# Optimization experiments

Hardware: AMD Instinct MI355X
Metric: run time of the kernel (lower is better)

## Reference

```python
import jax, jax.numpy as jnp
import numpy as np

N_NODES = 100000
N_EDGES = 1600000
N_GRAPHS = 1000
D_IN = 128
HID = 128
OUT = 6


def setup_inputs() -> dict:
    key = jax.random.key(0)
    ks = jax.random.split(key, 12)
    s = 1.0 / np.sqrt(HID)
    x = jax.random.normal(ks[0], (N_NODES, D_IN), dtype=jnp.float32)
    ei = jax.random.randint(ks[1], (2, N_EDGES), 0, N_NODES, dtype=jnp.int64)
    batch = jnp.sort(jax.random.randint(ks[2], (N_NODES,), 0, N_GRAPHS, dtype=jnp.int64))
    return {
        "x": x,
        "ei": ei,
        "batch": batch,
        "W1a": jax.random.normal(ks[3], (D_IN, HID), dtype=jnp.float32) * s,
        "b1a": jnp.zeros((HID,), jnp.float32),
        "W1b": jax.random.normal(ks[4], (HID, HID), dtype=jnp.float32) * s,
        "b1b": jnp.zeros((HID,), jnp.float32),
        "W2a": jax.random.normal(ks[5], (HID, HID), dtype=jnp.float32) * s,
        "b2a": jnp.zeros((HID,), jnp.float32),
        "W2b": jax.random.normal(ks[6], (HID, HID), dtype=jnp.float32) * s,
        "b2b": jnp.zeros((HID,), jnp.float32),
        "Wlin": jax.random.normal(ks[7], (HID, OUT), dtype=jnp.float32) * s,
        "blin": jnp.zeros((OUT,), jnp.float32),
    }


def _gin_conv(x, src, dst, Wa, ba, Wb, bb):
    # PyG GINConv (eps=0): mlp(x_i + sum_{j->i} x_j)
    agg = jax.ops.segment_sum(x[src], dst, num_segments=N_NODES)
    h = agg + x
    h = jnp.maximum(h @ Wa + ba, 0.0)
    return h @ Wb + bb


def reference(x, ei, batch, W1a, b1a, W1b, b1b, W2a, b2a, W2b, b2b, Wlin, blin):
    src, dst = ei[0], ei[1]
    h = jnp.maximum(_gin_conv(x, src, dst, W1a, b1a, W1b, b1b), 0.0)
    # dropout is identity in eval mode
    h = _gin_conv(h, src, dst, W2a, b2a, W2b, b2b)
    # global mean pool per graph
    sums = jax.ops.segment_sum(h, batch, num_segments=N_GRAPHS)
    cnts = jax.ops.segment_sum(jnp.ones((h.shape[0], 1), h.dtype), batch, num_segments=N_GRAPHS)
    pooled = sums / jnp.maximum(cnts, 1.0)
    return pooled @ Wlin + blin
```

## Files before the change

kernel.cpp:

```cpp
#include <hip/hip_runtime.h>

#define N_NODES 100000
#define N_EDGES 1600000
#define N_GRAPHS 1000
#define HID 128
#define OUTD 6

#define BUCK_LOG 7
#define BUCK_W (1 << BUCK_LOG)
#define NBUCK ((N_NODES + BUCK_W - 1) >> BUCK_LOG)
#define BCAP 2560
#define FILL_BLOCKS 512
#define FILL_CHUNK 3128

#define CVT_BLOCKS 6250
#define GST_BLOCKS 391
#define PACK_BLOCKS 32
#define PREP_BLOCKS (CVT_BLOCKS + GST_BLOCKS + PACK_BLOCKS + FILL_BLOCKS)

typedef _Float16 h2 __attribute__((ext_vector_type(2)));
typedef _Float16 half8 __attribute__((ext_vector_type(8)));
typedef float f32x4 __attribute__((ext_vector_type(4)));

__global__ __launch_bounds__(256) void k_prep(const float* __restrict__ x,
                                              const int* __restrict__ batch,
                                              const int* __restrict__ srcv,
                                              const int* __restrict__ dstv,
                                              const float* __restrict__ W1a,
                                              const float* __restrict__ W1b,
                                              const float* __restrict__ W2a,
                                              const float* __restrict__ W2b,
                                              _Float16* __restrict__ X16,
                                              int* __restrict__ gstart,
                                              _Float16* __restrict__ P,
                                              int* __restrict__ bcur0,
                                              int* __restrict__ packed) {
    __shared__ int h[NBUCK];
    __shared__ int lcur[NBUCK];
    __shared__ int dcache[FILL_CHUNK];
    int b = blockIdx.x, t = threadIdx.x;
    if (b < FILL_BLOCKS) {
        int e0 = b * FILL_CHUNK;
        int e1 = min(e0 + FILL_CHUNK, N_EDGES);
        for (int i = t; i < NBUCK; i += 256) h[i] = 0;
        __syncthreads();
        int ev = e0 + ((e1 - e0) & ~3);
        for (int e = e0 + t * 4; e < ev; e += 1024) {
            int4 d4 = *(const int4*)(dstv + e);
            *(int4*)&dcache[e - e0] = d4;
            atomicAdd(&h[d4.x >> BUCK_LOG], 1);
            atomicAdd(&h[d4.y >> BUCK_LOG], 1);
            atomicAdd(&h[d4.z >> BUCK_LOG], 1);
            atomicAdd(&h[d4.w >> BUCK_LOG], 1);
        }
        for (int e = ev + t; e < e1; e += 256) {
            int d = dstv[e];
            dcache[e - e0] = d;
            atomicAdd(&h[d >> BUCK_LOG], 1);
        }
        __syncthreads();
        for (int i = t; i < NBUCK; i += 256) {
            int c = h[i];
            lcur[i] = c ? atomicAdd(&bcur0[i], c) : 0;
        }
        __syncthreads();
        for (int e = e0 + t * 4; e < ev; e += 1024) {
            int4 d4 = *(const int4*)&dcache[e - e0];
            int4 s4 = *(const int4*)(srcv + e);
            int b0 = d4.x >> BUCK_LOG, b1 = d4.y >> BUCK_LOG;
            int b2 = d4.z >> BUCK_LOG, b3 = d4.w >> BUCK_LOG;
            int p0 = atomicAdd(&lcur[b0], 1);
            int p1 = atomicAdd(&lcur[b1], 1);
            int p2 = atomicAdd(&lcur[b2], 1);
            int p3 = atomicAdd(&lcur[b3], 1);
            if (p0 < BCAP) packed[b0 * BCAP + p0] = ((d4.x & (BUCK_W - 1)) << 20) | s4.x;
            if (p1 < BCAP) packed[b1 * BCAP + p1] = ((d4.y & (BUCK_W - 1)) << 20) | s4.y;
            if (p2 < BCAP) packed[b2 * BCAP + p2] = ((d4.z & (BUCK_W - 1)) << 20) | s4.z;
            if (p3 < BCAP) packed[b3 * BCAP + p3] = ((d4.w & (BUCK_W - 1)) << 20) | s4.w;
        }
        for (int e = ev + t; e < e1; e += 256) {
            int d = dcache[e - e0];
            int bk = d >> BUCK_LOG;
            int pos = atomicAdd(&lcur[bk], 1);
            if (pos < BCAP) packed[bk * BCAP + pos] = ((d & (BUCK_W - 1)) << 20) | srcv[e];
        }
    } else if (b < FILL_BLOCKS + CVT_BLOCKS) {
        size_t i = ((size_t)(b - FILL_BLOCKS) * 256 + t) * 8;
        float4 v0 = *(const float4*)(x + i);
        float4 v1 = *(const float4*)(x + i + 4);
        half8 o;
        o[0] = (_Float16)v0.x; o[1] = (_Float16)v0.y; o[2] = (_Float16)v0.z; o[3] = (_Float16)v0.w;
        o[4] = (_Float16)v1.x; o[5] = (_Float16)v1.y; o[6] = (_Float16)v1.z; o[7] = (_Float16)v1.w;
        *(half8*)(X16 + i) = o;
    } else if (b < FILL_BLOCKS + CVT_BLOCKS + GST_BLOCKS) {
        int n = (b - FILL_BLOCKS - CVT_BLOCKS) * 256 + t;
        if (n < N_NODES) {
            int bb = batch[n];
            int prev = (n == 0) ? -1 : batch[n - 1];
            for (int g = prev + 1; g <= bb; ++g) gstart[g] = n;
            if (n == N_NODES - 1)
                for (int g = bb + 1; g <= N_GRAPHS; ++g) gstart[g] = N_NODES;
        }
    } else {
        int gid = (b - FILL_BLOCKS - CVT_BLOCKS - GST_BLOCKS) * 256 + t;
        int mat = gid >> 11;
        int r = gid & 2047;
        int ctks = r >> 6;
        int lane = r & 63;
        int col = (ctks >> 2) * 16 + (lane & 15);
        int k0 = (ctks & 3) * 32 + (lane >> 4) * 8;
        const float* W = (mat == 0) ? W1a : (mat == 1) ? W1b : (mat == 2) ? W2a : W2b;
        _Float16* dp = P + mat * 16384 + r * 8;
#pragma unroll
        for (int j = 0; j < 8; ++j) dp[j] = (_Float16)W[(k0 + j) * HID + col];
    }
}

__global__ __launch_bounds__(256) void k_csrfine(const int* __restrict__ packed,
                                                 const int* __restrict__ bcur0,
                                                 int* __restrict__ offsets,
                                                 int* __restrict__ csr_src) {
    __shared__ int hist[BUCK_W];
    __shared__ int scan[BUCK_W];
    __shared__ int cur[BUCK_W];
    __shared__ int red[4];
    int b = blockIdx.x;
    int base = b << BUCK_LOG;
    int t = threadIdx.x;
    int partial = 0;
    for (int j = t; j < b; j += 256) partial += bcur0[j];
#pragma unroll
    for (int d = 32; d > 0; d >>= 1) partial += __shfl_down(partial, d, 64);
    if ((t & 63) == 0) red[t >> 6] = partial;
    __syncthreads();
    int s = red[0] + red[1] + red[2] + red[3];
    int cnt = bcur0[b];
    if (cnt > BCAP) cnt = BCAP;
    const int* pb = packed + b * BCAP;

    if (t < BUCK_W) hist[t] = 0;
    __syncthreads();
    for (int i = t; i < cnt; i += 256) atomicAdd(&hist[pb[i] >> 20], 1);
    __syncthreads();
    if (t < BUCK_W) scan[t] = hist[t];
    __syncthreads();
    for (int d = 1; d < BUCK_W; d <<= 1) {
        int a = 0;
        if (t >= d && t < BUCK_W) a = scan[t - d];
        __syncthreads();
        if (t < BUCK_W) scan[t] += a;
        __syncthreads();
    }
    if (t < BUCK_W) {
        int node = base + t;
        if (node < N_NODES) {
            int excl = scan[t] - hist[t];
            offsets[node] = s + excl;
            cur[t] = excl;
        }
    }
    if (b == 0 && t == 0) offsets[N_NODES] = N_EDGES;
    __syncthreads();
    for (int i = t; i < cnt; i += 256) {
        int v = pb[i];
        int ln = v >> 20;
        int pos = atomicAdd(&cur[ln], 1);
        csr_src[s + pos] = v & 0xFFFFF;
    }
}

static __device__ __forceinline__ half8 shfl_xor_h8(half8 v, int mask) {
    union { half8 h; int i[4]; } a, b;
    a.h = v;
#pragma unroll
    for (int k = 0; k < 4; ++k) b.i[k] = __shfl_xor(a.i[k], mask, 64);
    return b.h;
}

__global__ __launch_bounds__(256) void k_gather16(const _Float16* __restrict__ x,
                                                  const int* __restrict__ csr,
                                                  const int* __restrict__ offs,
                                                  _Float16* __restrict__ out) {
    int t = threadIdx.x;
    int wave = t >> 6, lane = t & 63;
    int g = lane >> 4;
    int l = lane & 15;
    int node = __builtin_amdgcn_readfirstlane(blockIdx.x * 4 + wave);
    const half8* xp8 = (const half8*)x;
    int s = offs[node], e = offs[node + 1];

    half8 z = {0, 0, 0, 0, 0, 0, 0, 0};
    half8 acc0 = (g == 0) ? xp8[(size_t)node * 16 + l] : z;
    half8 acc1 = z;

    for (int base = s; base < e; base += 64) {
        int cnt = e - base;
        if (cnt > 64) cnt = 64;
        int myidx = (base + lane < e) ? csr[base + lane] : 0;
        int j = 0;
        for (; j + 16 <= cnt; j += 16) {
            int i0 = __shfl(myidx, j + g, 64);
            int i1 = __shfl(myidx, j + 4 + g, 64);
            int i2 = __shfl(myidx, j + 8 + g, 64);
            int i3 = __shfl(myidx, j + 12 + g, 64);
            acc0 += xp8[(size_t)i0 * 16 + l];
            acc1 += xp8[(size_t)i1 * 16 + l];
            acc0 += xp8[(size_t)i2 * 16 + l];
            acc1 += xp8[(size_t)i3 * 16 + l];
        }
        for (; j < cnt; j += 4) {
            int sl = j + g;
            int idx = __shfl(myidx, sl < cnt ? sl : 0, 64);
            if (sl < cnt) acc0 += xp8[(size_t)idx * 16 + l];
        }
    }
    half8 r = acc0 + acc1;
    r += shfl_xor_h8(r, 16);
    r += shfl_xor_h8(r, 32);
    if (g == 0) ((half8*)out)[(size_t)node * 16 + l] = r;
}

static __device__ __forceinline__ unsigned long long pack4(float v0, float v1,
                                                           float v2, float v3) {
    union { h2 h[2]; unsigned long long u; } u;
    h2 p0, p1;
    p0[0] = (_Float16)v0; p0[1] = (_Float16)v1;
    p1[0] = (_Float16)v2; p1[1] = (_Float16)v3;
    u.h[0] = p0; u.h[1] = p1;
    return u.u;
}

template <int RELU_OUT>
__global__ __launch_bounds__(256, 2) void k_mlp16(const _Float16* __restrict__ in,
                                                  const _Float16* __restrict__ Wap,
                                                  const float* __restrict__ ba,
                                                  const _Float16* __restrict__ Wbp,
                                                  const float* __restrict__ bb,
                                                  _Float16* __restrict__ out) {
    __shared__ uint4 WaS4[2048];
    __shared__ uint4 WbS4[2048];
    __shared__ unsigned long long hS[4][512];
    int t = threadIdx.x;
    int wave = t >> 6, lane = t & 63;
    int l = lane & 15, w = lane >> 4;
    int row0 = blockIdx.x * 256 + wave * 64;

    const uint4* wa4 = (const uint4*)Wap;
    const uint4* wb4 = (const uint4*)Wbp;
#pragma unroll
    for (int i = 0; i < 8; ++i) WaS4[t + i * 256] = wa4[t + i * 256];
#pragma unroll
    for (int i = 0; i < 8; ++i) WbS4[t + i * 256] = wb4[t + i * 256];
    __syncthreads();
    const half8* waf = (const half8*)WaS4;
    const half8* wbf = (const half8*)WbS4;
    unsigned long long* h64 = hS[wave];
    int swz = ((l & 3) << 2) ^ (((l >> 2) & 1) << 1);

    float4 baR[8], bbR[8];
#pragma unroll
    for (int ct = 0; ct < 8; ++ct) {
        baR[ct] = *(const float4*)(ba + ct * 16 + w * 4);
        bbR[ct] = *(const float4*)(bb + ct * 16 + w * 4);
    }

#pragma unroll
    for (int tile = 0; tile < 4; ++tile) {
        int row = row0 + tile * 16 + l;
        bool rok = row < N_NODES;
        const _Float16* rp = in + (size_t)row * HID + w * 8;
        half8 xf[4];
#pragma unroll
        for (int ks = 0; ks < 4; ++ks) {
            half8 v = {0, 0, 0, 0, 0, 0, 0, 0};
            if (rok) v = *(const half8*)(rp + ks * 32);
            xf[ks] = v;
        }
#pragma unroll
        for (int ct = 0; ct < 8; ++ct) {
            f32x4 c = {0.f, 0.f, 0.f, 0.f};
#pragma unroll
            for (int ks = 0; ks < 4; ++ks)
                c = __builtin_amdgcn_mfma_f32_16x16x32_f16(waf[(ct * 4 + ks) * 64 + lane],
                                                           xf[ks], c, 0, 0, 0);
            float4 b4 = baR[ct];
            h64[l * 32 + ((ct * 4 + w) ^ swz)] =
                pack4(fmaxf(c[0] + b4.x, 0.f), fmaxf(c[1] + b4.y, 0.f),
                      fmaxf(c[2] + b4.z, 0.f), fmaxf(c[3] + b4.w, 0.f));
        }
        half8 hf[4];
#pragma unroll
        for (int ks = 0; ks < 4; ++ks) {
            int slot = (ks * 8 + w * 2) ^ swz;
            hf[ks] = *(const half8*)&h64[l * 32 + slot];
        }
#pragma unroll
        for (int ct = 0; ct < 8; ++ct) {
            f32x4 c = {0.f, 0.f, 0.f, 0.f};
#pragma unroll
            for (int ks = 0; ks < 4; ++ks)
                c = __builtin_amdgcn_mfma_f32_16x16x32_f16(wbf[(ct * 4 + ks) * 64 + lane],
                                                           hf[ks], c, 0, 0, 0);
            float4 b4 = bbR[ct];
            float v0 = c[0] + b4.x, v1 = c[1] + b4.y, v2 = c[2] + b4.z, v3 = c[3] + b4.w;
            if (RELU_OUT) {
                v0 = fmaxf(v0, 0.f); v1 = fmaxf(v1, 0.f);
                v2 = fmaxf(v2, 0.f); v3 = fmaxf(v3, 0.f);
            }
            if (rok)
                *(unsigned long long*)(out + (size_t)row * HID + ct * 16 + w * 4) =
                    pack4(v0, v1, v2, v3);
        }
    }
}

__global__ __launch_bounds__(256) void k_pool_head(const _Float16* __restrict__ h,
                                                   const int* __restrict__ gstart,
                                                   const float* __restrict__ Wlin,
                                                   const float* __restrict__ blin,
                                                   float* __restrict__ out) {
    __shared__ float sums[4][HID];
    int g = blockIdx.x;
    int t = threadIdx.x;
    int wave = t >> 6, lane = t & 63;
    int s = gstart[g], e = gstart[g + 1];
    float ax = 0.f, ay = 0.f;
    const h2* hp = (const h2*)h;
    int r = s + wave;
    for (; r + 12 < e; r += 16) {
        h2 v0 = hp[(size_t)r * 64 + lane];
        h2 v1 = hp[(size_t)(r + 4) * 64 + lane];
        h2 v2 = hp[(size_t)(r + 8) * 64 + lane];
        h2 v3 = hp[(size_t)(r + 12) * 64 + lane];
        ax += (float)v0[0] + (float)v1[0] + (float)v2[0] + (float)v3[0];
        ay += (float)v0[1] + (float)v1[1] + (float)v2[1] + (float)v3[1];
    }
    for (; r < e; r += 4) {
        h2 v = hp[(size_t)r * 64 + lane];
        ax += (float)v[0];
        ay += (float)v[1];
    }
    sums[wave][2 * lane] = ax;
    sums[wave][2 * lane + 1] = ay;
    __syncthreads();
    if (wave != 0) return;
    float c = fmaxf((float)(e - s), 1.0f);
    float px = (sums[0][2 * lane] + sums[1][2 * lane] + sums[2][2 * lane] + sums[3][2 * lane]) / c;
    float py = (sums[0][2 * lane + 1] + sums[1][2 * lane + 1] + sums[2][2 * lane + 1] +
                sums[3][2 * lane + 1]) / c;
#pragma unroll
    for (int o = 0; o < OUTD; ++o) {
        float v = px * Wlin[(2 * lane) * OUTD + o] + py * Wlin[(2 * lane + 1) * OUTD + o];
#pragma unroll
        for (int d = 32; d > 0; d >>= 1) v += __shfl_down(v, d, 64);
        if (lane == 0) out[g * OUTD + o] = v + blin[o];
    }
}

extern "C" void kernel_launch(void* const* d_in, const int* in_sizes, int n_in,
                              void* d_out, int out_size, void* d_ws, size_t ws_size,
                              hipStream_t stream) {
    const float* x    = (const float*)d_in[0];
    const int*   ei   = (const int*)d_in[1];
    const int*   batch= (const int*)d_in[2];
    const float* W1a  = (const float*)d_in[3];
    const float* b1a  = (const float*)d_in[4];
    const float* W1b  = (const float*)d_in[5];
    const float* b1b  = (const float*)d_in[6];
    const float* W2a  = (const float*)d_in[7];
    const float* b2a  = (const float*)d_in[8];
    const float* W2b  = (const float*)d_in[9];
    const float* b2b  = (const float*)d_in[10];
    const float* Wlin = (const float*)d_in[11];
    const float* blin = (const float*)d_in[12];
    const int* src = ei;
    const int* dst = ei + N_EDGES;
    float* out = (float*)d_out;

    char* ws = (char*)d_ws;
    size_t off = 0;
    auto alloc = [&](size_t bytes) -> void* {
        void* p = ws + off;
        off += (bytes + 255) & ~(size_t)255;
        return p;
    };
    _Float16* X16 = (_Float16*)alloc(2ull * N_NODES * HID);
    _Float16* M   = (_Float16*)alloc(2ull * N_NODES * HID + 65536);
    _Float16* H1  = (_Float16*)alloc(2ull * N_NODES * HID + 65536);
    int*   csr_src = (int*)alloc(sizeof(int) * (size_t)N_EDGES);
    int*   offsets = (int*)alloc(sizeof(int) * (N_NODES + 1));
    int*   gstart  = (int*)alloc(sizeof(int) * (N_GRAPHS + 1));
    int*   bcur0   = (int*)alloc(sizeof(int) * NBUCK);
    _Float16* Wpack = (_Float16*)alloc(2ull * 4 * 16384);
    int* packed = (int*)H1;
    _Float16* M2 = M;
    _Float16* H2 = X16;
    (void)ws_size; (void)in_sizes; (void)n_in; (void)out_size;

    hipMemsetAsync(bcur0, 0, sizeof(int) * NBUCK, stream);

    k_prep<<<PREP_BLOCKS, 256, 0, stream>>>(x, batch, src, dst, W1a, W1b, W2a, W2b,
                                            X16, gstart, Wpack, bcur0, packed);
    k_csrfine<<<NBUCK, 256, 0, stream>>>(packed, bcur0, offsets, csr_src);

    k_gather16<<<N_NODES / 4, 256, 0, stream>>>(X16, csr_src, offsets, M);
    k_mlp16<1><<<(N_NODES + 255) / 256, 256, 0, stream>>>(M, Wpack + 0 * 16384, b1a,
                                                          Wpack + 1 * 16384, b1b, H1);
    k_gather16<<<N_NODES / 4, 256, 0, stream>>>(H1, csr_src, offsets, M2);
    k_mlp16<0><<<(N_NODES + 255) / 256, 256, 0, stream>>>(M2, Wpack + 2 * 16384, b2a,
                                                          Wpack + 3 * 16384, b2b, H2);

    k_pool_head<<<N_GRAPHS, 256, 0, stream>>>(H2, gstart, Wlin, blin, out);
}
```

Before: 306.9 us.

## Fuse second GIN MLP with mean-pool via per-graph atomic accumulation

Replaces the second MLP kernel and the pooling kernel with a fused kernel that computes the layer-2 MLP and sums each row's output into a per-graph fp32 buffer. Tiles whose 16 rows share one graph are reduced with shuffles before a single atomic per column; mixed tiles fall back to per-row atomics. A small head kernel then divides by counts and applies the linear layer. This removes the write and re-read of the 100k x 128 fp16 H2 tensor. In exchange it adds atomic traffic, a larger memset and nondeterministic summation order.

```diff
diff --git a/kernel.cpp b/kernel.cpp
--- a/kernel.cpp
+++ b/kernel.cpp
@@ -314,40 +314,127 @@
     }
 }
 
-__global__ __launch_bounds__(256) void k_pool_head(const _Float16* __restrict__ h,
-                                                   const int* __restrict__ gstart,
-                                                   const float* __restrict__ Wlin,
-                                                   const float* __restrict__ blin,
-                                                   float* __restrict__ out) {
-    __shared__ float sums[4][HID];
-    int g = blockIdx.x;
+__global__ __launch_bounds__(256, 2) void k_mlp2pool(const _Float16* __restrict__ in,
+                                                     const _Float16* __restrict__ Wap,
+                                                     const float* __restrict__ ba,
+                                                     const _Float16* __restrict__ Wbp,
+                                                     const float* __restrict__ bb,
+                                                     const int* __restrict__ batch,
+                                                     float* __restrict__ pooled) {
+    __shared__ uint4 WaS4[2048];
+    __shared__ uint4 WbS4[2048];
+    __shared__ unsigned long long hS[4][512];
     int t = threadIdx.x;
     int wave = t >> 6, lane = t & 63;
+    int l = lane & 15, w = lane >> 4;
+    int row0 = blockIdx.x * 256 + wave * 64;
+
+    const uint4* wa4 = (const uint4*)Wap;
+    const uint4* wb4 = (const uint4*)Wbp;
+#pragma unroll
+    for (int i = 0; i < 8; ++i) WaS4[t + i * 256] = wa4[t + i * 256];
+#pragma unroll
+    for (int i = 0; i < 8; ++i) WbS4[t + i * 256] = wb4[t + i * 256];
+    __syncthreads();
+    const half8* waf = (const half8*)WaS4;
+    const half8* wbf = (const half8*)WbS4;
+    unsigned long long* h64 = hS[wave];
+    int swz = ((l & 3) << 2) ^ (((l >> 2) & 1) << 1);
+
+    float4 baR[8], bbR[8];
+#pragma unroll
+    for (int ct = 0; ct < 8; ++ct) {
+        baR[ct] = *(const float4*)(ba + ct * 16 + w * 4);
+        bbR[ct] = *(const float4*)(bb + ct * 16 + w * 4);
+    }
+
+#pragma unroll
+    for (int tile = 0; tile < 4; ++tile) {
+        int row = row0 + tile * 16 + l;
+        bool rok = row < N_NODES;
+        int rowc = rok ? row : (N_NODES - 1);
+        int g = batch[rowc];
+        int mn = g, mx = g;
+#pragma unroll
+        for (int m = 1; m < 16; m <<= 1) {
+            mn = min(mn, __shfl_xor(mn, m, 64));
+            mx = max(mx, __shfl_xor(mx, m, 64));
+        }
+        bool uni = (mn == mx);
+
+        const _Float16* rp = in + (size_t)row * HID + w * 8;
+        half8 xf[4];
+#pragma unroll
+        for (int ks = 0; ks < 4; ++ks) {
+            half8 v = {0, 0, 0, 0, 0, 0, 0, 0};
+            if (rok) v = *(const half8*)(rp + ks * 32);
+            xf[ks] = v;
+        }
+#pragma unroll
+        for (int ct = 0; ct < 8; ++ct) {
+            f32x4 c = {0.f, 0.f, 0.f, 0.f};
+#pragma unroll
+            for (int ks = 0; ks < 4; ++ks)
+                c = __builtin_amdgcn_mfma_f32_16x16x32_f16(waf[(ct * 4 + ks) * 64 + lane],
+                                                           xf[ks], c, 0, 0, 0);
+            float4 b4 = baR[ct];
+            h64[l * 32 + ((ct * 4 + w) ^ swz)] =
+                pack4(fmaxf(c[0] + b4.x, 0.f), fmaxf(c[1] + b4.y, 0.f),
+                      fmaxf(c[2] + b4.z, 0.f), fmaxf(c[3] + b4.w, 0.f));
+        }
+        half8 hf[4];
+#pragma unroll
+        for (int ks = 0; ks < 4; ++ks) {
+            int slot = (ks * 8 + w * 2) ^ swz;
+            hf[ks] = *(const half8*)&h64[l * 32 + slot];
+        }
+#pragma unroll
+        for (int ct = 0; ct < 8; ++ct) {
+            f32x4 c = {0.f, 0.f, 0.f, 0.f};
+#pragma unroll
+            for (int ks = 0; ks < 4; ++ks)
+                c = __builtin_amdgcn_mfma_f32_16x16x32_f16(wbf[(ct * 4 + ks) * 64 + lane],
+                                                           hf[ks], c, 0, 0, 0);
+            float4 b4 = bbR[ct];
+            float v0 = c[0] + b4.x, v1 = c[1] + b4.y, v2 = c[2] + b4.z, v3 = c[3] + b4.w;
+            if (!rok) { v0 = 0.f; v1 = 0.f; v2 = 0.f; v3 = 0.f; }
+            if (uni) {
+#pragma unroll
+                for (int m = 1; m < 16; m <<= 1) {
+                    v0 += __shfl_xor(v0, m, 64);
+                    v1 += __shfl_xor(v1, m, 64);
+                    v2 += __shfl_xor(v2, m, 64);
+                    v3 += __shfl_xor(v3, m, 64);
+                }
+                if (l == 0) {
+                    float* pp = pooled + (size_t)g * HID + ct * 16 + w * 4;
+                    atomicAdd(pp + 0, v0);
+                    atomicAdd(pp + 1, v1);
+                    atomicAdd(pp + 2, v2);
+                    atomicAdd(pp + 3, v3);
+                }
+            } else if (rok) {
+                float* pp = pooled + (size_t)g * HID + ct * 16 + w * 4;
+                atomicAdd(pp + 0, v0);
+                atomicAdd(pp + 1, v1);
+                atomicAdd(pp + 2, v2);
+                atomicAdd(pp + 3, v3);
+            }
+        }
+    }
+}
+
+__global__ __launch_bounds__(64) void k_head(const float* __restrict__ pooled,
+                                             const int* __restrict__ gstart,
+                                             const float* __restrict__ Wlin,
+                                             const float* __restrict__ blin,
+                                             float* __restrict__ out) {
+    int g = blockIdx.x;
+    int lane = threadIdx.x;
     int s = gstart[g], e = gstart[g + 1];
-    float ax = 0.f, ay = 0.f;
-    const h2* hp = (const h2*)h;
-    int r = s + wave;
-    for (; r + 12 < e; r += 16) {
-        h2 v0 = hp[(size_t)r * 64 + lane];
-        h2 v1 = hp[(size_t)(r + 4) * 64 + lane];
-        h2 v2 = hp[(size_t)(r + 8) * 64 + lane];
-        h2 v3 = hp[(size_t)(r + 12) * 64 + lane];
-        ax += (float)v0[0] + (float)v1[0] + (float)v2[0] + (float)v3[0];
-        ay += (float)v0[1] + (float)v1[1] + (float)v2[1] + (float)v3[1];
-    }
-    for (; r < e; r += 4) {
-        h2 v = hp[(size_t)r * 64 + lane];
-        ax += (float)v[0];
-        ay += (float)v[1];
-    }
-    sums[wave][2 * lane] = ax;
-    sums[wave][2 * lane + 1] = ay;
-    __syncthreads();
-    if (wave != 0) return;
     float c = fmaxf((float)(e - s), 1.0f);
-    float px = (sums[0][2 * lane] + sums[1][2 * lane] + sums[2][2 * lane] + sums[3][2 * lane]) / c;
-    float py = (sums[0][2 * lane + 1] + sums[1][2 * lane + 1] + sums[2][2 * lane + 1] +
-                sums[3][2 * lane + 1]) / c;
+    float px = pooled[(size_t)g * HID + 2 * lane] / c;
+    float py = pooled[(size_t)g * HID + 2 * lane + 1] / c;
 #pragma unroll
     for (int o = 0; o < OUTD; ++o) {
         float v = px * Wlin[(2 * lane) * OUTD + o] + py * Wlin[(2 * lane + 1) * OUTD + o];
@@ -390,14 +477,14 @@
     int*   csr_src = (int*)alloc(sizeof(int) * (size_t)N_EDGES);
     int*   offsets = (int*)alloc(sizeof(int) * (N_NODES + 1));
     int*   gstart  = (int*)alloc(sizeof(int) * (N_GRAPHS + 1));
-    int*   bcur0   = (int*)alloc(sizeof(int) * NBUCK);
+    int*   bcur0   = (int*)alloc(sizeof(int) * NBUCK + sizeof(float) * N_GRAPHS * HID);
+    float* pooled  = (float*)(bcur0 + NBUCK);
     _Float16* Wpack = (_Float16*)alloc(2ull * 4 * 16384);
     int* packed = (int*)H1;
     _Float16* M2 = M;
-    _Float16* H2 = X16;
     (void)ws_size; (void)in_sizes; (void)n_in; (void)out_size;
 
-    hipMemsetAsync(bcur0, 0, sizeof(int) * NBUCK, stream);
+    hipMemsetAsync(bcur0, 0, sizeof(int) * NBUCK + sizeof(float) * N_GRAPHS * HID, stream);
 
     k_prep<<<PREP_BLOCKS, 256, 0, stream>>>(x, batch, src, dst, W1a, W1b, W2a, W2b,
                                             X16, gstart, Wpack, bcur0, packed);
@@ -407,8 +494,8 @@
     k_mlp16<1><<<(N_NODES + 255) / 256, 256, 0, stream>>>(M, Wpack + 0 * 16384, b1a,
                                                           Wpack + 1 * 16384, b1b, H1);
     k_gather16<<<N_NODES / 4, 256, 0, stream>>>(H1, csr_src, offsets, M2);
-    k_mlp16<0><<<(N_NODES + 255) / 256, 256, 0, stream>>>(M2, Wpack + 2 * 16384, b2a,
-                                                          Wpack + 3 * 16384, b2b, H2);
-
-    k_pool_head<<<N_GRAPHS, 256, 0, stream>>>(H2, gstart, Wlin, blin, out);
-}
+    k_mlp2pool<<<(N_NODES + 255) / 256, 256, 0, stream>>>(M2, Wpack + 2 * 16384, b2a,
+                                                          Wpack + 3 * 16384, b2b, batch, pooled);
+
+    k_head<<<N_GRAPHS, 64, 0, stream>>>(pooled, gstart, Wlin, blin, out);
+}
```

Result: slower. 447.0 us (+45.7%).
